# Performance work log

Measured on AMD Instinct MI355X. Metric: run time of the kernel, lower is better.

Reference implementation:

```python
import jax, jax.numpy as jnp
import numpy as np

LEAKY_SLOPE = 0.01  # torch F.leaky_relu default


def _l2norm(x):
    # matches F.normalize(p=2, dim=-1, eps=1e-12)
    n = jnp.linalg.norm(x, axis=-1, keepdims=True)
    return x / jnp.maximum(n, 1e-12)


def setup_inputs() -> dict:
    key = jax.random.key(0)
    k1, k2, k3, k4 = jax.random.split(key, 4)
    B, S, H = 16, 256, 768
    return {
        "query_embs": jax.random.normal(k1, (B, S, H), dtype=jnp.float32),
        "key_embs": jax.random.normal(k2, (2 * B, S, H), dtype=jnp.float32),
        "logit_scale": jnp.log(jnp.asarray(1.0 / 0.07, dtype=jnp.float32)),
        "alpha_raw": jnp.asarray(1.0, dtype=jnp.float32),
        "q_mask": jax.random.randint(k3, (B, S), 0, 2).astype(jnp.int32),
        "k_mask": jax.random.randint(k4, (2 * B, S), 0, 2).astype(jnp.int32),
    }


def reference(query_embs, key_embs, logit_scale, alpha_raw, q_mask, k_mask):
    q = _l2norm(query_embs)                 # [B, S, H]
    k = _l2norm(key_embs)                   # [2B, S, H]
    S = q.shape[1]

    # all-pairs token similarity: [B, 2B, S, S]
    sim = jnp.einsum('ish,jth->ijst', q, k)

    # exponential distance weighting
    pos = jnp.arange(S)
    dist = jnp.abs(pos[:, None] - pos[None, :]).astype(sim.dtype)
    alpha = jax.nn.leaky_relu(alpha_raw, LEAKY_SLOPE)
    sim = sim * jnp.exp(-alpha * dist)

    # joint validity mask: q_mask[i,s] & k_mask[j,t]
    valid = (q_mask[:, None, :, None] * k_mask[None, :, None, :]) > 0

    logits = jnp.where(valid, jnp.exp(logit_scale) * sim, -jnp.inf)
    p = jnp.nan_to_num(jax.nn.softmax(logits, axis=-1), nan=0.0)  # fully-masked rows -> 0

    # softmax-weighted aggregation of key tokens, then dot with query tokens
    agg = jnp.einsum('ijst,jth->ijsh', p, k)        # [B, 2B, S, H]
    per_tok = jnp.einsum('ish,ijsh->ijs', q, agg)   # [B, 2B, S]
    per_tok = per_tok * q_mask[:, None, :].astype(per_tok.dtype)
    return per_tok.sum(axis=-1)                     # [B, 2B]
```

## Files before the change

### kernel.cpp

```cpp
#include <hip/hip_runtime.h>
#include <hip/hip_bf16.h>

#define BQ   16
#define BK2  32
#define SEQ  256
#define HD   768

typedef __attribute__((ext_vector_type(8))) short bf16x8;
typedef __attribute__((ext_vector_type(4))) float f32x4;

__device__ __forceinline__ void glds16(const unsigned short* g, unsigned short* l) {
    __builtin_amdgcn_global_load_lds(
        (const __attribute__((address_space(1))) unsigned int*)g,
        (__attribute__((address_space(3))) unsigned int*)l, 16, 0, 0);
}

__device__ __forceinline__ unsigned int pack2_bf16(float a, float b) {
    unsigned ua = __float_as_uint(a), ub = __float_as_uint(b);
    ua += 0x7FFFu + ((ua >> 16) & 1u);
    ub += 0x7FFFu + ((ub >> 16) & 1u);
    return (ua >> 16) | (ub & 0xFFFF0000u);
}

__global__ __launch_bounds__(256) void norm_kernel(
    const float* __restrict__ q, const float* __restrict__ k,
    unsigned short* __restrict__ qn, unsigned short* __restrict__ kn,
    float* __restrict__ out)
{
    if (blockIdx.x == 0 && threadIdx.x < 256) {
        out[threadIdx.x] = 0.f; out[threadIdx.x + 256] = 0.f;
    }
    int row  = blockIdx.x * 4 + (threadIdx.x >> 6);
    int lane = threadIdx.x & 63;
    const int NQ = BQ * SEQ;
    const float* src = (row < NQ) ? q + (size_t)row * HD
                                  : k + (size_t)(row - NQ) * HD;
    unsigned int* dst = (unsigned int*)((row < NQ) ? qn + (size_t)row * HD
                                                   : kn + (size_t)(row - NQ) * HD);
    float4 v[3];
    float ss = 0.f;
#pragma unroll
    for (int c = 0; c < 3; ++c) {
        v[c] = ((const float4*)src)[lane + 64 * c];
        ss += v[c].x * v[c].x + v[c].y * v[c].y + v[c].z * v[c].z + v[c].w * v[c].w;
    }
#pragma unroll
    for (int m = 1; m < 64; m <<= 1) ss += __shfl_xor(ss, m, 64);
    float inv = rsqrtf(fmaxf(ss, 1e-24f));
#pragma unroll
    for (int c = 0; c < 3; ++c) {
        uint2 o = make_uint2(pack2_bf16(v[c].x * inv, v[c].y * inv),
                             pack2_bf16(v[c].z * inv, v[c].w * inv));
        ((uint2*)dst)[lane + 64 * c] = o;
    }
}

__global__ __launch_bounds__(64) void comp_kernel(
    const int* __restrict__ q_mask, const int* __restrict__ k_mask,
    int* __restrict__ sidx, int* __restrict__ cnts,
    int* __restrict__ tidx, int* __restrict__ cntt)
{
    const int row  = blockIdx.x;
    const int lane = threadIdx.x;
    const bool isq = row < BQ;
    const int* m = isq ? q_mask + row * SEQ : k_mask + (row - BQ) * SEQ;
    int* idx     = isq ? sidx + row * SEQ  : tidx + (row - BQ) * SEQ;
    int base = 0;
#pragma unroll
    for (int c = 0; c < 4; ++c) {
        int v = (m[c * 64 + lane] != 0);
        unsigned long long b = __ballot(v);
        int pre = __popcll(b & ((1ull << lane) - 1ull));
        if (v) idx[base + pre] = c * 64 + lane;
        base += (int)__popcll(b);
    }
    for (int p = base + lane; p < SEQ; p += 64) idx[p] = 0;
    if (lane == 0) { if (isq) cnts[row] = base; else cntt[row - BQ] = base; }
}

__global__ __launch_bounds__(512, 2) void li_kernel(
    const unsigned short* __restrict__ qn, const unsigned short* __restrict__ kn,
    const float* __restrict__ g_ls, const float* __restrict__ g_ar,
    const int* __restrict__ sidx, const int* __restrict__ cnts,
    const int* __restrict__ tidx, const int* __restrict__ cntt,
    float* __restrict__ out)
{
    const int j  = blockIdx.x, i = blockIdx.y, chs = blockIdx.z;
    const int cs = cnts[i], ct = cntt[j];
    if (chs * 128 >= cs || ct == 0) return;
    const int ntg = (ct + 63) >> 6;

    const int tid  = threadIdx.x;
    const int w    = tid >> 6, lane = tid & 63;
    const int ln   = lane & 15, lg = lane >> 4;
    const int wsd  = w >> 2, wt = w & 3;

    __shared__ __align__(16) unsigned short As[128 * 64];
    __shared__ __align__(16) unsigned short Bs[256 * 64];
    __shared__ float w2[SEQ];
    __shared__ int   sor[128], tor[SEQ];
    __shared__ float red[8];

    float a0 = g_ar[0];
    float alpha = (a0 > 0.f) ? a0 : 0.01f * a0;
    float scale = __expf(g_ls[0]) * 1.4426950408889634f;
    if (tid < 256) {
        w2[tid]  = scale * __expf(-alpha * (float)tid);
        tor[tid] = tidx[j * SEQ + tid];
    } else if (tid < 384) {
        sor[tid - 256] = sidx[i * SEQ + chs * 128 + (tid - 256)];
    }

    const int rl  = lane >> 3;
    const int gch = (lane & 7) ^ rl;
    const int ia0 = sidx[i * SEQ + chs * 128 + w * 8 + rl];
    const int ia1 = sidx[i * SEQ + chs * 128 + 64 + w * 8 + rl];
    int ib[4];
#pragma unroll
    for (int c = 0; c < 4; ++c)
        ib[c] = tidx[j * SEQ + c * 64 + w * 8 + rl];
    const unsigned short* qb = qn + (size_t)i * SEQ * HD + gch * 8;
    const unsigned short* kb = kn + (size_t)j * SEQ * HD + gch * 8;
    unsigned short* al = As + (w * 8) * 64;
    unsigned short* bl = Bs + (w * 8) * 64;

    f32x4 acc[4][4];
    const f32x4 zero4 = {0.f, 0.f, 0.f, 0.f};
#pragma unroll
    for (int a = 0; a < 4; ++a)
#pragma unroll
        for (int b = 0; b < 4; ++b) acc[a][b] = zero4;

    const bool wact = (wt < ntg);

    for (int kk = 0; kk < HD; kk += 64) {
        __syncthreads();
        glds16(qb + (size_t)ia0 * HD + kk, al);
        glds16(qb + (size_t)ia1 * HD + kk, al + 64 * 64);
#pragma unroll
        for (int c = 0; c < 4; ++c)
            if (c < ntg) glds16(kb + (size_t)ib[c] * HD + kk, bl + c * (64 * 64));
        __syncthreads();
        if (wact) {
            const bf16x8* A8 = (const bf16x8*)As;
            const bf16x8* B8 = (const bf16x8*)Bs;
#pragma unroll
            for (int ks = 0; ks < 2; ++ks) {
                const int ch = (ks * 4 + lg) ^ (ln & 7);
                bf16x8 af[4], bfr[4];
#pragma unroll
                for (int rm = 0; rm < 4; ++rm)
                    af[rm] = A8[(wsd * 64 + rm * 16 + ln) * 8 + ch];
#pragma unroll
                for (int cn = 0; cn < 4; ++cn)
                    bfr[cn] = B8[(wt * 64 + cn * 16 + ln) * 8 + ch];
#pragma unroll
                for (int rm = 0; rm < 4; ++rm)
#pragma unroll
                    for (int cn = 0; cn < 4; ++cn)
                        acc[rm][cn] = __builtin_amdgcn_mfma_f32_16x16x32_bf16(
                            af[rm], bfr[cn], acc[rm][cn], 0, 0, 0);
            }
        }
    }

    __syncthreads();
    float* zs  = (float*)Bs;
    float* wsc = zs + 16 * 133;

    int   to[4];
    float kv[4];
#pragma unroll
    for (int cn = 0; cn < 4; ++cn) {
        int slot = wt * 64 + cn * 16 + ln;
        to[cn] = tor[slot];
        kv[cn] = (slot < ct) ? 1.f : 0.f;
    }

#pragma unroll
    for (int rm = 0; rm < 4; ++rm)
#pragma unroll
        for (int r = 0; r < 4; ++r) {
            int srow = wsd * 64 + rm * 16 + lg * 4 + r;
            float ze = 0.f, we = 0.f;
            if (wact) {
                int so = sor[srow];
#pragma unroll
                for (int cn = 0; cn < 4; ++cn) {
                    float sim = acc[rm][cn][r];
                    int d = so - to[cn]; d = (d < 0) ? -d : d;
                    float e = kv[cn] * __builtin_exp2f(sim * w2[d]);
                    ze += e;
                    we = fmaf(e, sim, we);
                }
            }
            ze += __shfl_xor(ze, 1, 64);  we += __shfl_xor(we, 1, 64);
            ze += __shfl_xor(ze, 2, 64);  we += __shfl_xor(we, 2, 64);
            if ((ln & 3) == 0) {
                int zrow = wt * 4 + (ln >> 2);
                zs [zrow * 133 + srow] = ze;
                wsc[zrow * 133 + srow] = we;
            }
        }
    __syncthreads();

    float part = 0.f;
    if (tid < 128) {
        float Z = 0.f, W = 0.f;
#pragma unroll
        for (int c = 0; c < 16; ++c) {
            Z += zs [c * 133 + tid];
            W += wsc[c * 133 + tid];
        }
        float pt = (Z > 0.f) ? (W / Z) : 0.f;
        part = (chs * 128 + tid < cs) ? pt : 0.f;
    }
#pragma unroll
    for (int m = 1; m < 64; m <<= 1) part += __shfl_xor(part, m, 64);
    if (lane == 0) red[w] = part;
    __syncthreads();
    if (tid == 0) {
        float tot = red[0] + red[1] + red[2] + red[3]
                  + red[4] + red[5] + red[6] + red[7];
        atomicAdd(&out[i * BK2 + j], tot);
    }
}

extern "C" void kernel_launch(void* const* d_in, const int* in_sizes, int n_in,
                              void* d_out, int out_size, void* d_ws, size_t ws_size,
                              hipStream_t stream) {
    const float* q  = (const float*)d_in[0];
    const float* k  = (const float*)d_in[1];
    const float* ls = (const float*)d_in[2];
    const float* ar = (const float*)d_in[3];
    const int* qm   = (const int*)d_in[4];
    const int* km   = (const int*)d_in[5];
    float* out      = (float*)d_out;

    unsigned short* qn = (unsigned short*)d_ws;
    unsigned short* kn = qn + (size_t)BQ * SEQ * HD;
    int* sidx = (int*)(kn + (size_t)BK2 * SEQ * HD);
    int* cnts = sidx + BQ * SEQ;
    int* tidx = cnts + BQ;
    int* cntt = tidx + BK2 * SEQ;

    norm_kernel<<<(BQ + BK2) * SEQ / 4, 256, 0, stream>>>(q, k, qn, kn, (float*)d_out);
    comp_kernel<<<BQ + BK2, 64, 0, stream>>>(qm, km, sidx, cnts, tidx, cntt);
    li_kernel<<<dim3(BK2, BQ, 2), 512, 0, stream>>>(qn, kn, ls, ar,
                                                    sidx, cnts, tidx, cntt,
                                                    (float*)d_out);
}
```

Before: 132.0 us.

## Fuse mask compaction into norm kernel and skip empty MFMA tiles

Moves the mask-compaction work into 12 extra blocks of the normalization kernel, which removes one kernel launch. In the similarity GEMM, each wave now works out how many 16-row and 16-column tiles actually hold valid tokens. It skips MFMAs and LDS fragment loads for tiles that are fully padded, and skips the second A-tile global load when the chunk has 64 or fewer rows. This adds branching and a partial-tile code path in exchange for less wasted matrix work given the roughly 50% masks.

```diff
diff --git a/kernel.cpp b/kernel.cpp
--- a/kernel.cpp
+++ b/kernel.cpp
@@ -25,13 +25,37 @@
 __global__ __launch_bounds__(256) void norm_kernel(
     const float* __restrict__ q, const float* __restrict__ k,
     unsigned short* __restrict__ qn, unsigned short* __restrict__ kn,
+    const int* __restrict__ q_mask, const int* __restrict__ k_mask,
+    int* __restrict__ sidx, int* __restrict__ cnts,
+    int* __restrict__ tidx, int* __restrict__ cntt,
     float* __restrict__ out)
 {
+    const int w    = threadIdx.x >> 6;
+    const int lane = threadIdx.x & 63;
+
+    if (blockIdx.x >= 3072) {
+        const int row48 = (blockIdx.x - 3072) * 4 + w;
+        const bool isq = row48 < BQ;
+        const int* m = isq ? q_mask + row48 * SEQ : k_mask + (row48 - BQ) * SEQ;
+        int* idx     = isq ? sidx + row48 * SEQ  : tidx + (row48 - BQ) * SEQ;
+        int base = 0;
+#pragma unroll
+        for (int c = 0; c < 4; ++c) {
+            int v = (m[c * 64 + lane] != 0);
+            unsigned long long b = __ballot(v);
+            int pre = __popcll(b & ((1ull << lane) - 1ull));
+            if (v) idx[base + pre] = c * 64 + lane;
+            base += (int)__popcll(b);
+        }
+        for (int p = base + lane; p < SEQ; p += 64) idx[p] = 0;
+        if (lane == 0) { if (isq) cnts[row48] = base; else cntt[row48 - BQ] = base; }
+        return;
+    }
+
     if (blockIdx.x == 0 && threadIdx.x < 256) {
         out[threadIdx.x] = 0.f; out[threadIdx.x + 256] = 0.f;
     }
-    int row  = blockIdx.x * 4 + (threadIdx.x >> 6);
-    int lane = threadIdx.x & 63;
+    int row  = blockIdx.x * 4 + w;
     const int NQ = BQ * SEQ;
     const float* src = (row < NQ) ? q + (size_t)row * HD
                                   : k + (size_t)(row - NQ) * HD;
@@ -53,29 +77,6 @@
                              pack2_bf16(v[c].z * inv, v[c].w * inv));
         ((uint2*)dst)[lane + 64 * c] = o;
     }
-}
-
-__global__ __launch_bounds__(64) void comp_kernel(
-    const int* __restrict__ q_mask, const int* __restrict__ k_mask,
-    int* __restrict__ sidx, int* __restrict__ cnts,
-    int* __restrict__ tidx, int* __restrict__ cntt)
-{
-    const int row  = blockIdx.x;
-    const int lane = threadIdx.x;
-    const bool isq = row < BQ;
-    const int* m = isq ? q_mask + row * SEQ : k_mask + (row - BQ) * SEQ;
-    int* idx     = isq ? sidx + row * SEQ  : tidx + (row - BQ) * SEQ;
-    int base = 0;
-#pragma unroll
-    for (int c = 0; c < 4; ++c) {
-        int v = (m[c * 64 + lane] != 0);
-        unsigned long long b = __ballot(v);
-        int pre = __popcll(b & ((1ull << lane) - 1ull));
-        if (v) idx[base + pre] = c * 64 + lane;
-        base += (int)__popcll(b);
-    }
-    for (int p = base + lane; p < SEQ; p += 64) idx[p] = 0;
-    if (lane == 0) { if (isq) cnts[row] = base; else cntt[row - BQ] = base; }
 }
 
 __global__ __launch_bounds__(512, 2) void li_kernel(
@@ -88,12 +89,20 @@
     const int j  = blockIdx.x, i = blockIdx.y, chs = blockIdx.z;
     const int cs = cnts[i], ct = cntt[j];
     if (chs * 128 >= cs || ct == 0) return;
-    const int ntg = (ct + 63) >> 6;
+    int csrem = cs - chs * 128; if (csrem > 128) csrem = 128;
+    const int ns16 = (csrem + 15) >> 4;
+    const int nt16 = (ct + 15) >> 4;
+    const int ntg  = (nt16 + 3) >> 2;
 
     const int tid  = threadIdx.x;
     const int w    = tid >> 6, lane = tid & 63;
     const int ln   = lane & 15, lg = lane >> 4;
     const int wsd  = w >> 2, wt = w & 3;
+
+    int rmact = ns16 - wsd * 4; rmact = rmact < 0 ? 0 : (rmact > 4 ? 4 : rmact);
+    int cnact = nt16 - wt * 4;  cnact = cnact < 0 ? 0 : (cnact > 4 ? 4 : cnact);
+    const bool full = (rmact == 4) & (cnact == 4);
+    const bool wactive = (rmact > 0) & (cnact > 0);
 
     __shared__ __align__(16) unsigned short As[128 * 64];
     __shared__ __align__(16) unsigned short Bs[256 * 64];
@@ -123,6 +132,7 @@
     const unsigned short* kb = kn + (size_t)j * SEQ * HD + gch * 8;
     unsigned short* al = As + (w * 8) * 64;
     unsigned short* bl = Bs + (w * 8) * 64;
+    const bool stA1 = (csrem > 64);
 
     f32x4 acc[4][4];
     const f32x4 zero4 = {0.f, 0.f, 0.f, 0.f};
@@ -130,24 +140,22 @@
     for (int a = 0; a < 4; ++a)
 #pragma unroll
         for (int b = 0; b < 4; ++b) acc[a][b] = zero4;
-
-    const bool wact = (wt < ntg);
 
     for (int kk = 0; kk < HD; kk += 64) {
         __syncthreads();
         glds16(qb + (size_t)ia0 * HD + kk, al);
-        glds16(qb + (size_t)ia1 * HD + kk, al + 64 * 64);
+        if (stA1) glds16(qb + (size_t)ia1 * HD + kk, al + 64 * 64);
 #pragma unroll
         for (int c = 0; c < 4; ++c)
             if (c < ntg) glds16(kb + (size_t)ib[c] * HD + kk, bl + c * (64 * 64));
         __syncthreads();
-        if (wact) {
-            const bf16x8* A8 = (const bf16x8*)As;
-            const bf16x8* B8 = (const bf16x8*)Bs;
-#pragma unroll
-            for (int ks = 0; ks < 2; ++ks) {
-                const int ch = (ks * 4 + lg) ^ (ln & 7);
-                bf16x8 af[4], bfr[4];
+        const bf16x8* A8 = (const bf16x8*)As;
+        const bf16x8* B8 = (const bf16x8*)Bs;
+#pragma unroll
+        for (int ks = 0; ks < 2; ++ks) {
+            const int ch = (ks * 4 + lg) ^ (ln & 7);
+            bf16x8 af[4], bfr[4];
+            if (full) {
 #pragma unroll
                 for (int rm = 0; rm < 4; ++rm)
                     af[rm] = A8[(wsd * 64 + rm * 16 + ln) * 8 + ch];
@@ -160,6 +168,20 @@
                     for (int cn = 0; cn < 4; ++cn)
                         acc[rm][cn] = __builtin_amdgcn_mfma_f32_16x16x32_bf16(
                             af[rm], bfr[cn], acc[rm][cn], 0, 0, 0);
+            } else if (wactive) {
+#pragma unroll
+                for (int rm = 0; rm < 4; ++rm)
+                    if (rm < rmact) af[rm] = A8[(wsd * 64 + rm * 16 + ln) * 8 + ch];
+#pragma unroll
+                for (int cn = 0; cn < 4; ++cn)
+                    if (cn < cnact) bfr[cn] = B8[(wt * 64 + cn * 16 + ln) * 8 + ch];
+#pragma unroll
+                for (int rm = 0; rm < 4; ++rm)
+#pragma unroll
+                    for (int cn = 0; cn < 4; ++cn)
+                        if (rm < rmact && cn < cnact)
+                            acc[rm][cn] = __builtin_amdgcn_mfma_f32_16x16x32_bf16(
+                                af[rm], bfr[cn], acc[rm][cn], 0, 0, 0);
             }
         }
     }
@@ -183,7 +205,7 @@
         for (int r = 0; r < 4; ++r) {
             int srow = wsd * 64 + rm * 16 + lg * 4 + r;
             float ze = 0.f, we = 0.f;
-            if (wact) {
+            if (wactive) {
                 int so = sor[srow];
 #pragma unroll
                 for (int cn = 0; cn < 4; ++cn) {
@@ -244,8 +266,8 @@
     int* tidx = cnts + BQ;
     int* cntt = tidx + BK2 * SEQ;
 
-    norm_kernel<<<(BQ + BK2) * SEQ / 4, 256, 0, stream>>>(q, k, qn, kn, (float*)d_out);
-    comp_kernel<<<BQ + BK2, 64, 0, stream>>>(qm, km, sidx, cnts, tidx, cntt);
+    norm_kernel<<<(BQ + BK2) * SEQ / 4 + 12, 256, 0, stream>>>(
+        q, k, qn, kn, qm, km, sidx, cnts, tidx, cntt, (float*)d_out);
     li_kernel<<<dim3(BK2, BQ, 2), 512, 0, stream>>>(qn, kn, ls, ar,
                                                     sidx, cnts, tidx, cntt,
                                                     (float*)d_out);
```

New measurement: 148.7 us. +12.7%, slower.
